# Performance work log

Measured on AMD Instinct MI355X. Metric: run time of the kernel, lower is better.

The kernel has to match this reference:

```python
import jax, jax.numpy as jnp
import numpy as np

OUT_FEATURES = 4096
IN_FEATURES = 4096
NNZ = 1048576
BATCH = 128


def setup_inputs() -> dict:
    key = jax.random.key(0)
    k_x, k_v, k_r, k_c = jax.random.split(key, 4)
    X = jax.random.normal(k_x, (BATCH, IN_FEATURES), dtype=jnp.float32)
    W_vals = jax.random.normal(k_v, (NNZ,), dtype=jnp.float32)
    W_rows = jax.random.randint(k_r, (NNZ,), 0, OUT_FEATURES, dtype=jnp.int32)
    W_cols = jax.random.randint(k_c, (NNZ,), 0, IN_FEATURES, dtype=jnp.int32)
    return {"X": X, "W_vals": W_vals, "W_rows": W_rows, "W_cols": W_cols}


def reference(X, W_vals, W_rows, W_cols):
    # torch.sparse.mm(W, X.T).T with W in COO form.
    # out[b, i] = sum_{k: rows[k]==i} vals[k] * X[b, cols[k]]
    gathered = X.T[W_cols] * W_vals[:, None]            # [nnz, B]
    out_T = jax.ops.segment_sum(gathered, W_rows, num_segments=OUT_FEATURES)  # [OUT, B]
    return out_T.T                                       # [B, OUT]
```

## Files before the change

### kernel.cpp

```cpp
#include <hip/hip_runtime.h>
#include <hip/hip_bf16.h>

#define OUTF 4096
#define INF  4096
#define BATCH 128
#define NBIN 1024
#define NCELL 1024
#define CAP  16
#define SQ   1028

typedef _Float16 f16x8 __attribute__((ext_vector_type(8)));
typedef float    f32x4 __attribute__((ext_vector_type(4)));


__global__ __launch_bounds__(256) void k_prep(const float* __restrict__ X,
                                              const float* __restrict__ vals,
                                              const int* __restrict__ rows,
                                              const int* __restrict__ cols, int nnz,
                                              _Float16* __restrict__ Xh,
                                              int2* __restrict__ bucket,
                                              int* __restrict__ cnts) {
  __shared__ int cnt[NBIN];
  const int t = threadIdx.x;
  const int blk = blockIdx.x;
  if (blk < NCELL) {
    for (int b = t; b < NBIN; b += 256) cnt[b] = 0;
    __syncthreads();
    const int G4 = nnz >> 2;
    const int g = blk * 256 + t;
    if (g < G4) {
      int4   r4 = ((const int4*)rows)[g];
      int4   c4 = ((const int4*)cols)[g];
      float4 v4 = ((const float4*)vals)[g];
      int rr[4] = {r4.x, r4.y, r4.z, r4.w};
      int cc[4] = {c4.x, c4.y, c4.z, c4.w};
      float vv[4] = {v4.x, v4.y, v4.z, v4.w};
#pragma unroll
      for (int j = 0; j < 4; ++j) {
        int bin = ((rr[j] >> 4) << 2) | (cc[j] >> 10);
        int slot = atomicAdd(&cnt[bin], 1);
        if (slot < CAP) {
          int2 e;
          e.x = __float_as_int(vv[j]);
          e.y = ((rr[j] & 15) << 10) | (cc[j] & 1023);
          bucket[((size_t)blk * NBIN + bin) * CAP + slot] = e;
        }
      }
    }
    if (blk == 0) {
      for (int i = (nnz & ~3) + t; i < nnz; i += 256) {
        int r = rows[i], c = cols[i];
        int bin = ((r >> 4) << 2) | (c >> 10);
        int slot = atomicAdd(&cnt[bin], 1);
        if (slot < CAP) {
          int2 e;
          e.x = __float_as_int(vals[i]);
          e.y = ((r & 15) << 10) | (c & 1023);
          bucket[((size_t)blk * NBIN + bin) * CAP + slot] = e;
        }
      }
    }
    __syncthreads();
    for (int b = t; b < NBIN; b += 256)
      cnts[(size_t)blk * NBIN + b] = min(cnt[b], CAP);
  } else {
    int g = (blk - NCELL) * 256 + t;
    int n = g >> 9;
    int k0 = (g & 511) * 8;
    float4 f0 = *(const float4*)(X + (size_t)n * INF + k0);
    float4 f1 = *(const float4*)(X + (size_t)n * INF + k0 + 4);
    f16x8 h;
    h[0] = (_Float16)f0.x; h[1] = (_Float16)f0.y;
    h[2] = (_Float16)f0.z; h[3] = (_Float16)f0.w;
    h[4] = (_Float16)f1.x; h[5] = (_Float16)f1.y;
    h[6] = (_Float16)f1.z; h[7] = (_Float16)f1.w;
    size_t idx = ((size_t)(k0 >> 5) * 8 + (n >> 4)) * 512 + (n & 15) * 32 + (k0 & 31);
    *(f16x8*)(Xh + idx) = h;
  }
}

__global__ __launch_bounds__(256, 2) void k_strip(const int2* __restrict__ bucket,
                                                  const int* __restrict__ cnts,
                                                  const _Float16* __restrict__ Xh,
                                                  float* __restrict__ outP) {
  __shared__ float strip[16 * SQ];
  const int t = threadIdx.x;
  const int bin = blockIdx.x;
  const int mt = bin >> 2, kq = bin & 3;

  {
    float4 z = {0.f, 0.f, 0.f, 0.f};
    const int nvec = 16 * SQ / 4;
    for (int j = t; j < nvec; j += 256) ((float4*)strip)[j] = z;
  }
  __syncthreads();

  for (int cc = t; cc < NCELL; cc += 256) {
    int cnt = cnts[(size_t)cc * NBIN + bin];
    const int2* cell = bucket + ((size_t)cc * NBIN + bin) * CAP;
    for (int j = 0; j < cnt; ++j) {
      int2 e = cell[j];
      atomicAdd(&strip[((e.y >> 10) & 15) * SQ + (e.y & 1023)], __int_as_float(e.x));
    }
  }
  __syncthreads();

  const int lane = t & 63, wid = t >> 6;
  const int lr = lane & 15, lg = lane >> 4;
  f32x4 acc[8] = {};
  for (int ktl = wid; ktl < 32; ktl += 4) {
    const int kt = kq * 32 + ktl;
    float4 alo = *(const float4*)&strip[lr * SQ + ktl * 32 + lg * 8];
    float4 ahi = *(const float4*)&strip[lr * SQ + ktl * 32 + lg * 8 + 4];
    f16x8 a;
    a[0] = (_Float16)alo.x; a[1] = (_Float16)alo.y;
    a[2] = (_Float16)alo.z; a[3] = (_Float16)alo.w;
    a[4] = (_Float16)ahi.x; a[5] = (_Float16)ahi.y;
    a[6] = (_Float16)ahi.z; a[7] = (_Float16)ahi.w;
    const _Float16* bp = Xh + (size_t)kt * 4096 + lr * 32 + lg * 8;
    f16x8 b[8];
#pragma unroll
    for (int nt = 0; nt < 8; ++nt) b[nt] = *(const f16x8*)(bp + nt * 512);
#pragma unroll
    for (int nt = 0; nt < 8; ++nt)
      acc[nt] = __builtin_amdgcn_mfma_f32_16x16x32_f16(a, b[nt], acc[nt], 0, 0, 0);
  }
  __syncthreads();

  float* red = strip;
#pragma unroll
  for (int nt = 0; nt < 8; ++nt)
#pragma unroll
    for (int i = 0; i < 4; ++i)
      red[wid * 2048 + (lg * 4 + i) * 128 + nt * 16 + lr] = acc[nt][i];
  __syncthreads();
  float* op = outP + (size_t)kq * (OUTF * BATCH) + (size_t)mt * 2048;
  for (int e = t; e < 2048; e += 256)
    op[e] = red[e] + red[2048 + e] + red[4096 + e] + red[6144 + e];
}

__global__ __launch_bounds__(1024) void k_merge(const float* __restrict__ outP,
                                                float* __restrict__ out) {
  __shared__ float t[32][33];
  int bbase = blockIdx.x * 32;
  int rbase = blockIdx.y * 32;
  size_t src = (size_t)(rbase + threadIdx.y) * 128 + bbase + threadIdx.x;
  float s = outP[src] + outP[(size_t)OUTF * BATCH + src] +
            outP[(size_t)2 * OUTF * BATCH + src] + outP[(size_t)3 * OUTF * BATCH + src];
  t[threadIdx.y][threadIdx.x] = s;
  __syncthreads();
  out[(size_t)(bbase + threadIdx.y) * OUTF + rbase + threadIdx.x] = t[threadIdx.x][threadIdx.y];
}

__global__ __launch_bounds__(256) void k_fallback(const float* __restrict__ X,
                                                  const float* __restrict__ vals,
                                                  const int* __restrict__ rows,
                                                  const int* __restrict__ cols, int n,
                                                  float* __restrict__ out) {
  int k = blockIdx.x * blockDim.x + threadIdx.x;
  if (k >= n) return;
  float v = vals[k];
  int r = rows[k], c = cols[k];
  for (int b = 0; b < BATCH; ++b)
    atomicAdd(&out[(size_t)b * OUTF + r], v * X[(size_t)b * INF + c]);
}

extern "C" void kernel_launch(void* const* d_in, const int* in_sizes, int n_in,
                              void* d_out, int out_size, void* d_ws, size_t ws_size,
                              hipStream_t stream) {
  const float* X  = (const float*)d_in[0];
  const float* Wv = (const float*)d_in[1];
  const int*   Wr = (const int*)d_in[2];
  const int*   Wc = (const int*)d_in[3];
  float* out = (float*)d_out;
  const int nnz = in_sizes[1];

  char* ws = (char*)d_ws;
  const size_t OFF_XH   = 0;
  const size_t OFF_BKT  = OFF_XH  + (size_t)BATCH * INF * 2;
  const size_t OFF_CNT  = OFF_BKT + (size_t)NCELL * NBIN * CAP * 8;
  const size_t OFF_OUTP = OFF_CNT + (size_t)NCELL * NBIN * 4;
  const size_t NEEDED   = OFF_OUTP + (size_t)4 * OUTF * BATCH * 4;

  if (ws_size < NEEDED) {
    hipMemsetAsync(d_out, 0, (size_t)out_size * 4, stream);
    k_fallback<<<dim3((nnz + 255) / 256), dim3(256), 0, stream>>>(X, Wv, Wr, Wc, nnz, out);
    return;
  }

  _Float16* Xh     = (_Float16*)(ws + OFF_XH);
  int2*     bucket = (int2*)(ws + OFF_BKT);
  int*      cnts   = (int*)(ws + OFF_CNT);
  float*    outP   = (float*)(ws + OFF_OUTP);

  k_prep<<<dim3(NCELL + 256), dim3(256), 0, stream>>>(X, Wv, Wr, Wc, nnz, Xh, bucket, cnts);
  k_strip<<<dim3(NBIN), dim3(256), 0, stream>>>(bucket, cnts, Xh, outP);
  k_merge<<<dim3(BATCH / 32, OUTF / 32), dim3(32, 32), 0, stream>>>(outP, out);
}
```

Measured before the change: 122.2 us.

## Replace fixed-capacity COO buckets with per-chunk counting sort and segment offsets

The preprocessing kernel previously scattered each nonzero into fixed 16-slot cells per (chunk, bin), which needed a very large sparse bucket array plus a dense count table. Now each 1024-element chunk builds a shared-memory histogram, prefix-scans it into segment starts, stages entries sorted by bin in shared memory, and writes them back contiguously. The strip kernel then walks the compacted segments using start/end offsets. This removes the capacity cap that could silently drop entries and cuts workspace traffic. The cost is an extra block-level scan and more synchronisation in the prep kernel.

```diff
diff --git a/kernel.cpp b/kernel.cpp
--- a/kernel.cpp
+++ b/kernel.cpp
@@ -5,8 +5,8 @@
 #define INF  4096
 #define BATCH 128
 #define NBIN 1024
-#define NCELL 1024
-#define CAP  16
+#define CHUNK 1024
+#define SEGP (NBIN + 1)
 #define SQ   1028
 
 typedef _Float16 f16x8 __attribute__((ext_vector_type(8)));
@@ -16,55 +16,86 @@
 __global__ __launch_bounds__(256) void k_prep(const float* __restrict__ X,
                                               const float* __restrict__ vals,
                                               const int* __restrict__ rows,
-                                              const int* __restrict__ cols, int nnz,
+                                              const int* __restrict__ cols,
+                                              int nnz, int nw,
                                               _Float16* __restrict__ Xh,
                                               int2* __restrict__ bucket,
-                                              int* __restrict__ cnts) {
-  __shared__ int cnt[NBIN];
+                                              int* __restrict__ segStart) {
+  __shared__ int  hist[NBIN];
+  __shared__ int  scanT[256];
+  __shared__ int2 stage[CHUNK];
   const int t = threadIdx.x;
   const int blk = blockIdx.x;
-  if (blk < NCELL) {
-    for (int b = t; b < NBIN; b += 256) cnt[b] = 0;
-    __syncthreads();
-    const int G4 = nnz >> 2;
-    const int g = blk * 256 + t;
-    if (g < G4) {
+
+  if (blk < nw) {
+    const int s = blk * CHUNK;
+    const int e = min(nnz, s + CHUNK);
+    const int cnt = e - s;
+    for (int b = t; b < NBIN; b += 256) hist[b] = 0;
+    __syncthreads();
+
+    int   bins[4], metas[4];
+    float vv[4];
+    int   nloc = 0;
+    if (s + 4 * t + 3 < e) {
+      int g = (s >> 2) + t;
       int4   r4 = ((const int4*)rows)[g];
       int4   c4 = ((const int4*)cols)[g];
       float4 v4 = ((const float4*)vals)[g];
       int rr[4] = {r4.x, r4.y, r4.z, r4.w};
       int cc[4] = {c4.x, c4.y, c4.z, c4.w};
-      float vv[4] = {v4.x, v4.y, v4.z, v4.w};
+      float vf[4] = {v4.x, v4.y, v4.z, v4.w};
 #pragma unroll
       for (int j = 0; j < 4; ++j) {
-        int bin = ((rr[j] >> 4) << 2) | (cc[j] >> 10);
-        int slot = atomicAdd(&cnt[bin], 1);
-        if (slot < CAP) {
-          int2 e;
-          e.x = __float_as_int(vv[j]);
-          e.y = ((rr[j] & 15) << 10) | (cc[j] & 1023);
-          bucket[((size_t)blk * NBIN + bin) * CAP + slot] = e;
-        }
+        bins[j]  = ((rr[j] >> 4) << 2) | (cc[j] >> 10);
+        metas[j] = ((rr[j] & 15) << 10) | (cc[j] & 1023);
+        vv[j] = vf[j];
+        atomicAdd(&hist[bins[j]], 1);
       }
-    }
-    if (blk == 0) {
-      for (int i = (nnz & ~3) + t; i < nnz; i += 256) {
+      nloc = 4;
+    } else {
+      for (int i = s + 4 * t; i < e; ++i) {
         int r = rows[i], c = cols[i];
-        int bin = ((r >> 4) << 2) | (c >> 10);
-        int slot = atomicAdd(&cnt[bin], 1);
-        if (slot < CAP) {
-          int2 e;
-          e.x = __float_as_int(vals[i]);
-          e.y = ((r & 15) << 10) | (c & 1023);
-          bucket[((size_t)blk * NBIN + bin) * CAP + slot] = e;
-        }
+        bins[nloc]  = ((r >> 4) << 2) | (c >> 10);
+        metas[nloc] = ((r & 15) << 10) | (c & 1023);
+        vv[nloc] = vals[i];
+        atomicAdd(&hist[bins[nloc]], 1);
+        ++nloc;
       }
     }
     __syncthreads();
-    for (int b = t; b < NBIN; b += 256)
-      cnts[(size_t)blk * NBIN + b] = min(cnt[b], CAP);
+
+    const int base = t * 4;
+    int l0 = hist[base], l1 = hist[base + 1], l2 = hist[base + 2], l3 = hist[base + 3];
+    int sum = l0 + l1 + l2 + l3;
+    scanT[t] = sum;
+    __syncthreads();
+    for (int off = 1; off < 256; off <<= 1) {
+      int u = (t >= off) ? scanT[t - off] : 0;
+      __syncthreads();
+      scanT[t] += u;
+      __syncthreads();
+    }
+    int excl = scanT[t] - sum;
+    int st0 = excl, st1 = excl + l0, st2 = st1 + l1, st3 = st2 + l2;
+    int* sp = segStart + (size_t)blk * SEGP + base;
+    sp[0] = st0; sp[1] = st1; sp[2] = st2; sp[3] = st3;
+    hist[base] = st0; hist[base + 1] = st1; hist[base + 2] = st2; hist[base + 3] = st3;
+    if (t == 255) segStart[(size_t)blk * SEGP + NBIN] = cnt;
+    __syncthreads();
+
+    for (int j = 0; j < nloc; ++j) {
+      int slot = atomicAdd(&hist[bins[j]], 1);
+      int2 ent;
+      ent.x = __float_as_int(vv[j]);
+      ent.y = metas[j];
+      stage[slot] = ent;
+    }
+    __syncthreads();
+
+    for (int i = t; i < cnt; i += 256) bucket[s + i] = stage[i];
   } else {
-    int g = (blk - NCELL) * 256 + t;
+    int g = (blk - nw) * 256 + t;
     int n = g >> 9;
     int k0 = (g & 511) * 8;
     float4 f0 = *(const float4*)(X + (size_t)n * INF + k0);
@@ -80,7 +111,8 @@
 }
 
 __global__ __launch_bounds__(256, 2) void k_strip(const int2* __restrict__ bucket,
-                                                  const int* __restrict__ cnts,
+                                                  const int* __restrict__ segStart,
+                                                  int nw,
                                                   const _Float16* __restrict__ Xh,
                                                   float* __restrict__ outP) {
   __shared__ float strip[16 * SQ];
@@ -95,11 +127,13 @@
   }
   __syncthreads();
 
-  for (int cc = t; cc < NCELL; cc += 256) {
-    int cnt = cnts[(size_t)cc * NBIN + bin];
-    const int2* cell = bucket + ((size_t)cc * NBIN + bin) * CAP;
-    for (int j = 0; j < cnt; ++j) {
-      int2 e = cell[j];
+  for (int cc = t; cc < nw; cc += 256) {
+    const int* sp = segStart + (size_t)cc * SEGP + bin;
+    int sbase = sp[0];
+    int send  = sp[1];
+    const int2* p = bucket + (size_t)cc * CHUNK;
+    for (int j = sbase; j < send; ++j) {
+      int2 e = p[j];
       atomicAdd(&strip[((e.y >> 10) & 15) * SQ + (e.y & 1023)], __int_as_float(e.x));
     }
   }
@@ -174,12 +208,13 @@
   const int*   Wc = (const int*)d_in[3];
   float* out = (float*)d_out;
   const int nnz = in_sizes[1];
+  const int nw = (nnz + CHUNK - 1) / CHUNK;
 
   char* ws = (char*)d_ws;
   const size_t OFF_XH   = 0;
   const size_t OFF_BKT  = OFF_XH  + (size_t)BATCH * INF * 2;
-  const size_t OFF_CNT  = OFF_BKT + (size_t)NCELL * NBIN * CAP * 8;
-  const size_t OFF_OUTP = OFF_CNT + (size_t)NCELL * NBIN * 4;
+  const size_t OFF_SEG  = OFF_BKT + (size_t)nw * CHUNK * 8;
+  const size_t OFF_OUTP = OFF_SEG + (size_t)nw * SEGP * 4;
   const size_t NEEDED   = OFF_OUTP + (size_t)4 * OUTF * BATCH * 4;
 
   if (ws_size < NEEDED) {
@@ -188,12 +223,12 @@
     return;
   }
 
-  _Float16* Xh     = (_Float16*)(ws + OFF_XH);
-  int2*     bucket = (int2*)(ws + OFF_BKT);
-  int*      cnts   = (int*)(ws + OFF_CNT);
-  float*    outP   = (float*)(ws + OFF_OUTP);
-
-  k_prep<<<dim3(NCELL + 256), dim3(256), 0, stream>>>(X, Wv, Wr, Wc, nnz, Xh, bucket, cnts);
-  k_strip<<<dim3(NBIN), dim3(256), 0, stream>>>(bucket, cnts, Xh, outP);
+  _Float16* Xh       = (_Float16*)(ws + OFF_XH);
+  int2*     bucket   = (int2*)(ws + OFF_BKT);
+  int*      segStart = (int*)(ws + OFF_SEG);
+  float*    outP     = (float*)(ws + OFF_OUTP);
+
+  k_prep<<<dim3(nw + 256), dim3(256), 0, stream>>>(X, Wv, Wr, Wc, nnz, nw, Xh, bucket, segStart);
+  k_strip<<<dim3(NBIN), dim3(256), 0, stream>>>(bucket, segStart, nw, Xh, outP);
   k_merge<<<dim3(BATCH / 32, OUTF / 32), dim3(32, 32), 0, stream>>>(outP, out);
 }
```

Measured after the change: 114.7 us. -6.1%, faster.
